# Performance work log

Hardware: AMD Instinct MI355X
Metric: run time of the kernel (lower is better)

The kernel has to match this reference:

```python
import jax, jax.numpy as jnp
import numpy as np

IN_G, OUT_G, IN_MEM, OUT_MEM, N_EMBED = 64, 64, 8, 8, 512
DIM_QUANT = IN_MEM * OUT_MEM  # 64
B = 8192


def setup_inputs() -> dict:
    key = jax.random.key(0)
    k1, k2, k3 = jax.random.split(key, 3)
    x = jax.random.normal(k1, (B, IN_G * IN_MEM), dtype=jnp.float32)
    # xavier-uniform-ish init for weight
    bound = float(np.sqrt(6.0 / (IN_MEM + OUT_MEM)))
    weight = jax.random.uniform(k2, (IN_G, OUT_G, IN_MEM, OUT_MEM), dtype=jnp.float32,
                                minval=-bound, maxval=bound)
    # VQ codebook, stored (dim, n_embed) as in rosinality Quantize
    embed = jax.random.normal(k3, (DIM_QUANT, N_EMBED), dtype=jnp.float32)
    return {"x": x, "weight": weight, "embed": embed, "use_qw": 1}


def _quantize(w_flat, embed):
    # w_flat: [G, dim]; embed: [dim, n_embed]
    # dist = ||w||^2 - 2 w@e + ||e||^2  (squared euclidean)
    dist = ((w_flat ** 2).sum(axis=1, keepdims=True)
            - 2.0 * (w_flat @ embed)
            + (embed ** 2).sum(axis=0, keepdims=True))
    idx = jnp.argmin(dist, axis=1)
    quant = jnp.take(embed.T, idx, axis=0)  # embed_code: embedding on embed.T
    return quant, idx


def reference(x, weight, embed, use_qw):
    in_g, out_g, in_mem, out_mem = weight.shape
    b = x.shape[0]
    xg = x.reshape(b, in_g, in_mem).transpose(1, 0, 2)  # [g, b, i]
    if use_qw:
        w_flat = weight.reshape(in_g * out_g, in_mem * out_mem)
        quant, _ = _quantize(w_flat, embed)
        quant = quant.reshape(weight.shape)
        diff = jnp.mean((jax.lax.stop_gradient(quant) - weight) ** 2)
        # straight-through estimator
        q_w = weight + jax.lax.stop_gradient(quant - weight)
    else:
        q_w = weight
        diff = None
    # permute(0,2,1,3).reshape -> [g, in_mem, out_g*out_mem]
    q_w = q_w.transpose(0, 2, 1, 3).reshape(in_g, in_mem, out_g * out_mem)
    # grouped matmul + stack + sum over groups == single einsum contraction over g and i
    res = jnp.einsum('gbi,gio->bo', xg, q_w)  # [b, out_g*out_mem]
    return (res, diff)
```

## Files before the change

kernel.cpp:

```cpp
#include <hip/hip_runtime.h>
#include <cstdint>

#define NEMB   512
#define DQ     64
#define NROWS  4096
#define BATCH  8192
#define KDIM   512
#define NDIM   512

#define VQ_BLOCKS   512
#define CONV_BLOCKS 2048

typedef __attribute__((ext_vector_type(8))) short bf16x8;
typedef __attribute__((ext_vector_type(4))) float floatx4;

__device__ __forceinline__ unsigned short f2bf(float f) {
    unsigned int u = __float_as_uint(f);
    u += 0x7fffu + ((u >> 16) & 1u);
    return (unsigned short)(u >> 16);
}

__device__ __forceinline__ void async16(const void* g, void* l) {
    __builtin_amdgcn_global_load_lds(
        (const __attribute__((address_space(1))) void*)g,
        (__attribute__((address_space(3))) void*)l, 16, 0, 0);
}

__global__ __launch_bounds__(256) void fused_prep_vq(
    const float* __restrict__ x,
    const float* __restrict__ weight,
    const float* __restrict__ embed,
    unsigned short* __restrict__ xb,
    unsigned short* __restrict__ wt,
    float* __restrict__ partials,
    const int* __restrict__ use_qw)
{
    const int t   = threadIdx.x;
    const int bid = blockIdx.x;

    if (bid >= VQ_BLOCKS) {
        const int gid = (bid - VQ_BLOCKS) * 256 + t;
#pragma unroll
        for (int it = 0; it < 2; ++it) {
            const int idx = gid + it * 524288;
            float4 v = reinterpret_cast<const float4*>(x)[idx];
            ushort4 o;
            o.x = f2bf(v.x); o.y = f2bf(v.y); o.z = f2bf(v.z); o.w = f2bf(v.w);
            reinterpret_cast<ushort4*>(xb)[idx] = o;
        }
        return;
    }

    const int wave = t >> 6;
    const int lane = t & 63;
    const int rblk = bid * 8;
    const bool qon = (use_qw[0] != 0);

    __shared__ float  wlds[8 * 64];
    __shared__ double e2lds[NEMB];
    __shared__ int    bidx_lds[8];

    if (t < 128)
        reinterpret_cast<float4*>(wlds)[t] =
            reinterpret_cast<const float4*>(weight + (size_t)rblk * 64)[t];

    {
        double s0 = 0.0, s1 = 0.0;
        for (int d = 0; d < DQ; ++d) {
            const float2 e = *reinterpret_cast<const float2*>(embed + d * NEMB + 2 * t);
            s0 = fma((double)e.x, (double)e.x, s0);
            s1 = fma((double)e.y, (double)e.y, s1);
        }
        e2lds[2 * t]     = s0;
        e2lds[2 * t + 1] = s1;
    }
    __syncthreads();

    if (qon) {
        const int j0 = lane * 8;
        const int r0 = wave * 2;

        double a0[8], a1[8];
#pragma unroll
        for (int c = 0; c < 8; ++c) { a0[c] = 0.0; a1[c] = 0.0; }

        for (int d = 0; d < DQ; ++d) {
            const float4 ea = *reinterpret_cast<const float4*>(embed + d * NEMB + j0);
            const float4 eb = *reinterpret_cast<const float4*>(embed + d * NEMB + j0 + 4);
            double ev[8];
            ev[0] = (double)ea.x; ev[1] = (double)ea.y; ev[2] = (double)ea.z; ev[3] = (double)ea.w;
            ev[4] = (double)eb.x; ev[5] = (double)eb.y; ev[6] = (double)eb.z; ev[7] = (double)eb.w;
            const double w0 = (double)wlds[r0 * 64 + d];
            const double w1 = (double)wlds[r0 * 64 + 64 + d];
#pragma unroll
            for (int c = 0; c < 8; ++c) a0[c] = fma(w0, ev[c], a0[c]);
#pragma unroll
            for (int c = 0; c < 8; ++c) a1[c] = fma(w1, ev[c], a1[c]);
        }

#pragma unroll
        for (int r = 0; r < 2; ++r) {
            double best = 1e300;
            int bi = 0;
#pragma unroll
            for (int c = 0; c < 8; ++c) {
                const double q = fma(-2.0, (r == 0 ? a0[c] : a1[c]), e2lds[j0 + c]);
                if (q < best) { best = q; bi = j0 + c; }
            }
#pragma unroll
            for (int off = 1; off < 64; off <<= 1) {
                const double ob = __shfl_xor(best, off, 64);
                const int    oi = __shfl_xor(bi,   off, 64);
                if (ob < best || (ob == best && oi < bi)) { best = ob; bi = oi; }
            }
            if (lane == 0) bidx_lds[r0 + r] = bi;
        }
    }
    __syncthreads();

    float dsum = 0.f;
    if (t < 64) {
        const int rloc = t >> 3, om = t & 7;
        const int row = rblk + rloc;
        const int g = row >> 6, og = row & 63;
        const int bidx = qon ? bidx_lds[rloc] : 0;
        alignas(16) unsigned short q8[8];
#pragma unroll
        for (int i = 0; i < 8; ++i) {
            const int d = i * 8 + om;
            const float wv = wlds[rloc * 64 + d];
            float qv;
            if (qon) {
                qv = embed[d * NEMB + bidx];
                const float df = qv - wv;
                dsum = fmaf(df, df, dsum);
            } else {
                qv = wv;
            }
            q8[i] = f2bf(qv);
        }
        *reinterpret_cast<int4*>(wt + (size_t)(og * 8 + om) * KDIM + g * 8) =
            *reinterpret_cast<const int4*>(q8);
    }
    if (wave == 0) {
#pragma unroll
        for (int off = 32; off > 0; off >>= 1) dsum += __shfl_down(dsum, off, 64);
        if (lane == 0) partials[bid] = dsum;
    }
}

__global__ __launch_bounds__(256) void gemm_kernel(
    const unsigned short* __restrict__ xb,
    const unsigned short* __restrict__ wt,
    float* __restrict__ out,
    const float* __restrict__ partials,
    float* diff_slot)
{
    __shared__ unsigned short As[128 * 64];
    __shared__ unsigned short Bs[64 * 64];

    const int tid  = threadIdx.x;
    const int wave = tid >> 6;
    const int lane = tid & 63;

    const int flat = blockIdx.x;
    const int xcd  = flat & 7;
    const int sub  = flat >> 3;
    const int nt   = sub & 7;
    const int mt   = xcd * 8 + (sub >> 3);
    const int m0 = mt * 128;
    const int n0 = nt * 64;
    const int wm = (wave >> 1) * 64;
    const int wn = (wave & 1) * 32;

    const int srow   = lane >> 3;
    const int schunk = (lane & 7) ^ srow;
    const int mrow = lane & 15;
    const int cq   = lane >> 4;

    floatx4 acc[4][2] = {};

    for (int k0 = 0; k0 < KDIM; k0 += 64) {
        __syncthreads();
#pragma unroll
        for (int c = 0; c < 4; ++c) {
            const int g = wave * 4 + c;
            const int row = g * 8 + srow;
            async16(xb + (size_t)(m0 + row) * KDIM + k0 + schunk * 8, (char*)As + g * 1024);
        }
#pragma unroll
        for (int c = 0; c < 2; ++c) {
            const int g = wave * 2 + c;
            const int row = g * 8 + srow;
            async16(wt + (size_t)(n0 + row) * KDIM + k0 + schunk * 8, (char*)Bs + g * 1024);
        }
        __syncthreads();

#pragma unroll
        for (int ks = 0; ks < 2; ++ks) {
            bf16x8 a[4], b[2];
#pragma unroll
            for (int i = 0; i < 4; ++i) {
                const int r = wm + i * 16 + mrow;
                const int c = ks * 4 + cq;
                a[i] = *reinterpret_cast<const bf16x8*>(&As[r * 64 + ((c ^ (r & 7)) * 8)]);
            }
#pragma unroll
            for (int j = 0; j < 2; ++j) {
                const int r = wn + j * 16 + mrow;
                const int c = ks * 4 + cq;
                b[j] = *reinterpret_cast<const bf16x8*>(&Bs[r * 64 + ((c ^ (r & 7)) * 8)]);
            }
#pragma unroll
            for (int i = 0; i < 4; ++i)
#pragma unroll
                for (int j = 0; j < 2; ++j)
                    acc[i][j] = __builtin_amdgcn_mfma_f32_16x16x32_bf16(a[i], b[j], acc[i][j], 0, 0, 0);
        }
    }

    const int col = lane & 15;
    const int rbase = (lane >> 4) * 4;
#pragma unroll
    for (int i = 0; i < 4; ++i)
#pragma unroll
        for (int j = 0; j < 2; ++j)
#pragma unroll
            for (int r = 0; r < 4; ++r) {
                const int mm = m0 + wm + i * 16 + rbase + r;
                const int nn = n0 + wn + j * 16 + col;
                out[(size_t)mm * NDIM + nn] = acc[i][j][r];
            }

    if (flat == 0 && wave == 0 && diff_slot) {
        float s = 0.f;
#pragma unroll
        for (int q = 0; q < 8; ++q) s += partials[lane + 64 * q];
#pragma unroll
        for (int off = 32; off > 0; off >>= 1) s += __shfl_down(s, off, 64);
        if (lane == 0) diff_slot[0] = s * (1.f / (NROWS * DQ));
    }
}

extern "C" void kernel_launch(void* const* d_in, const int* in_sizes, int n_in,
                              void* d_out, int out_size, void* d_ws, size_t ws_size,
                              hipStream_t stream)
{
    const float* x      = (const float*)d_in[0];
    const float* weight = (const float*)d_in[1];
    const float* embed  = (const float*)d_in[2];
    const int*   use_qw = (const int*)d_in[3];
    float* out = (float*)d_out;

    unsigned short* wt = (unsigned short*)d_ws;
    float* partials    = (float*)((char*)d_ws + (512u << 10));
    unsigned short* xb = (unsigned short*)((char*)d_ws + (1u << 20));

    float* diff_slot = (out_size > BATCH * NDIM) ? (out + (size_t)BATCH * NDIM) : nullptr;

    fused_prep_vq<<<VQ_BLOCKS + CONV_BLOCKS, 256, 0, stream>>>(
        x, weight, embed, xb, wt, partials, use_qw);
    gemm_kernel<<<512, 256, 0, stream>>>(xb, wt, out, partials, diff_slot);
}
```

Measured before the change: 100.0 us.

## Fuse fp32-to-bf16 conversion of x into GEMM A-tile loads

Removes the separate pass that converted x to bf16 in a workspace buffer. The GEMM now streams fp32 x tiles directly into LDS with async loads, using a 16-way XOR swizzle, and converts them to bf16 in registers before the MFMA. This drops one full read and write of x in bf16 and the extra blocks in the prep kernel. In exchange it doubles LDS footprint and global bytes for the A tile, and each N-tile block redoes the conversion (8x redundant reads of x).

```diff
diff --git a/kernel.cpp b/kernel.cpp
--- a/kernel.cpp
+++ b/kernel.cpp
@@ -8,8 +8,7 @@
 #define KDIM   512
 #define NDIM   512
 
-#define VQ_BLOCKS   512
-#define CONV_BLOCKS 2048
+#define VQ_BLOCKS 512
 
 typedef __attribute__((ext_vector_type(8))) short bf16x8;
 typedef __attribute__((ext_vector_type(4))) float floatx4;
@@ -26,31 +25,15 @@
         (__attribute__((address_space(3))) void*)l, 16, 0, 0);
 }
 
-__global__ __launch_bounds__(256) void fused_prep_vq(
-    const float* __restrict__ x,
+__global__ __launch_bounds__(256) void vq_kernel(
     const float* __restrict__ weight,
     const float* __restrict__ embed,
-    unsigned short* __restrict__ xb,
     unsigned short* __restrict__ wt,
     float* __restrict__ partials,
     const int* __restrict__ use_qw)
 {
-    const int t   = threadIdx.x;
-    const int bid = blockIdx.x;
-
-    if (bid >= VQ_BLOCKS) {
-        const int gid = (bid - VQ_BLOCKS) * 256 + t;
-#pragma unroll
-        for (int it = 0; it < 2; ++it) {
-            const int idx = gid + it * 524288;
-            float4 v = reinterpret_cast<const float4*>(x)[idx];
-            ushort4 o;
-            o.x = f2bf(v.x); o.y = f2bf(v.y); o.z = f2bf(v.z); o.w = f2bf(v.w);
-            reinterpret_cast<ushort4*>(xb)[idx] = o;
-        }
-        return;
-    }
-
+    const int t    = threadIdx.x;
+    const int bid  = blockIdx.x;
     const int wave = t >> 6;
     const int lane = t & 63;
     const int rblk = bid * 8;
@@ -150,13 +133,13 @@
 }
 
 __global__ __launch_bounds__(256) void gemm_kernel(
-    const unsigned short* __restrict__ xb,
+    const float* __restrict__ x,
     const unsigned short* __restrict__ wt,
     float* __restrict__ out,
     const float* __restrict__ partials,
     float* diff_slot)
 {
-    __shared__ unsigned short As[128 * 64];
+    __shared__ float          Asf[128 * 64];
     __shared__ unsigned short Bs[64 * 64];
 
     const int tid  = threadIdx.x;
@@ -173,8 +156,10 @@
     const int wm = (wave >> 1) * 64;
     const int wn = (wave & 1) * 32;
 
-    const int srow   = lane >> 3;
-    const int schunk = (lane & 7) ^ srow;
+    const int srowA = lane >> 4;
+    const int posA  = lane & 15;
+    const int srowB   = lane >> 3;
+    const int schunkB = (lane & 7) ^ srowB;
     const int mrow = lane & 15;
     const int cq   = lane >> 4;
 
@@ -183,16 +168,19 @@
     for (int k0 = 0; k0 < KDIM; k0 += 64) {
         __syncthreads();
 #pragma unroll
-        for (int c = 0; c < 4; ++c) {
-            const int g = wave * 4 + c;
-            const int row = g * 8 + srow;
-            async16(xb + (size_t)(m0 + row) * KDIM + k0 + schunk * 8, (char*)As + g * 1024);
+        for (int c = 0; c < 8; ++c) {
+            const int g = wave * 8 + c;
+            const int rloc = g * 4 + srowA;
+            const int cA = posA ^ (rloc & 15);
+            async16(x + (size_t)(m0 + rloc) * KDIM + k0 + cA * 4,
+                    (char*)Asf + g * 1024);
         }
 #pragma unroll
         for (int c = 0; c < 2; ++c) {
             const int g = wave * 2 + c;
-            const int row = g * 8 + srow;
-            async16(wt + (size_t)(n0 + row) * KDIM + k0 + schunk * 8, (char*)Bs + g * 1024);
+            const int rloc = g * 8 + srowB;
+            async16(wt + (size_t)(n0 + rloc) * KDIM + k0 + schunkB * 8,
+                    (char*)Bs + g * 1024);
         }
         __syncthreads();
 
@@ -202,8 +190,17 @@
 #pragma unroll
             for (int i = 0; i < 4; ++i) {
                 const int r = wm + i * 16 + mrow;
-                const int c = ks * 4 + cq;
-                a[i] = *reinterpret_cast<const bf16x8*>(&As[r * 64 + ((c ^ (r & 7)) * 8)]);
+                const int c0 = ks * 8 + cq * 2;
+                const floatx4 f0 = *reinterpret_cast<const floatx4*>(
+                    &Asf[r * 64 + ((c0 ^ (r & 15)) * 4)]);
+                const floatx4 f1 = *reinterpret_cast<const floatx4*>(
+                    &Asf[r * 64 + (((c0 + 1) ^ (r & 15)) * 4)]);
+                bf16x8 v;
+                v[0] = (short)f2bf(f0.x); v[1] = (short)f2bf(f0.y);
+                v[2] = (short)f2bf(f0.z); v[3] = (short)f2bf(f0.w);
+                v[4] = (short)f2bf(f1.x); v[5] = (short)f2bf(f1.y);
+                v[6] = (short)f2bf(f1.z); v[7] = (short)f2bf(f1.w);
+                a[i] = v;
             }
 #pragma unroll
             for (int j = 0; j < 2; ++j) {
@@ -254,11 +251,9 @@
 
     unsigned short* wt = (unsigned short*)d_ws;
     float* partials    = (float*)((char*)d_ws + (512u << 10));
-    unsigned short* xb = (unsigned short*)((char*)d_ws + (1u << 20));
 
     float* diff_slot = (out_size > BATCH * NDIM) ? (out + (size_t)BATCH * NDIM) : nullptr;
 
-    fused_prep_vq<<<VQ_BLOCKS + CONV_BLOCKS, 256, 0, stream>>>(
-        x, weight, embed, xb, wt, partials, use_qw);
-    gemm_kernel<<<512, 256, 0, stream>>>(xb, wt, out, partials, diff_slot);
-}
+    vq_kernel<<<VQ_BLOCKS, 256, 0, stream>>>(weight, embed, wt, partials, use_qw);
+    gemm_kernel<<<512, 256, 0, stream>>>(x, wt, out, partials, diff_slot);
+}
```

After: 105.3 us. 5.3% more time.
